# Optimization experiments

Hardware: AMD Instinct MI355X
Metric: run time of the kernel (lower is better)

The kernel has to match this reference:

```python
import jax, jax.numpy as jnp
import numpy as np

B, S, H = 2, 1024, 2048
NH, NKV, D = 16, 4, 128
E, K, F = 16, 2, 1408          # routed experts, top_k, moe_intermediate
FS = 1408                      # shared-expert intermediate (n_shared_experts=1)
EPS = 1e-5
RSF = 1.0                      # routed_scaling_factor


def rmsnorm(x, w):
    v = jnp.mean(jnp.square(x.astype(jnp.float32)), axis=-1, keepdims=True)
    return (x * jax.lax.rsqrt(v + EPS)).astype(x.dtype) * w


def rotate_half(x):
    x1, x2 = jnp.split(x, 2, axis=-1)
    return jnp.concatenate([-x2, x1], axis=-1)


def apply_rope(x, cos, sin):
    # x: [B,S,h,D]; cos/sin: [S,D]
    c = cos[None, :, None, :]
    s = sin[None, :, None, :]
    return x * c + rotate_half(x) * s


def setup_inputs() -> dict:
    key = jax.random.key(0)
    ks = jax.random.split(key, 16)
    sc = 0.02
    hidden_states = jax.random.normal(ks[0], (B, S, H), dtype=jnp.float32)
    # rotary embedding tables
    inv_freq = 1.0 / (10000.0 ** (np.arange(0, D, 2, dtype=np.float32) / D))
    ang = np.arange(S, dtype=np.float32)[:, None] * inv_freq[None, :]
    emb = np.concatenate([ang, ang], axis=-1)
    cos = jnp.asarray(np.cos(emb), dtype=jnp.float32)
    sin = jnp.asarray(np.sin(emb), dtype=jnp.float32)
    return {
        'hidden_states': hidden_states,
        'cos': cos,
        'sin': sin,
        'ln1_w': jnp.ones((H,), jnp.float32),
        'ln2_w': jnp.ones((H,), jnp.float32),
        'q_norm_w': jnp.ones((D,), jnp.float32),
        'k_norm_w': jnp.ones((D,), jnp.float32),
        'wq': jax.random.normal(ks[1], (H, NH * D), jnp.float32) * sc,
        'wk': jax.random.normal(ks[2], (H, NKV * D), jnp.float32) * sc,
        'wv': jax.random.normal(ks[3], (H, NKV * D), jnp.float32) * sc,
        'wo': jax.random.normal(ks[4], (NH * D, H), jnp.float32) * sc,
        'gate_w': jax.random.normal(ks[5], (E, H), jnp.float32) * sc,
        'expert_gate_up': jax.random.normal(ks[6], (E, H, 2 * F), jnp.float32) * sc,
        'expert_down': jax.random.normal(ks[7], (E, F, H), jnp.float32) * sc,
        'shared_gate_up': jax.random.normal(ks[8], (H, 2 * FS), jnp.float32) * sc,
        'shared_down': jax.random.normal(ks[9], (FS, H), jnp.float32) * sc,
    }


def silu_and_mul(gu):
    g, u = jnp.split(gu, 2, axis=-1)
    return jax.nn.silu(g) * u


def moe_block(tokens, gate_w, expert_gate_up, expert_down, shared_gate_up, shared_down):
    # tokens: [T,H]
    T = tokens.shape[0]
    router_logits = tokens.astype(jnp.float32) @ gate_w.T          # [T,E]
    probs = jax.nn.softmax(router_logits, axis=-1)
    topk_w, topk_ids = jax.lax.top_k(probs, K)                     # [T,K]
    topk_w = topk_w / jnp.sum(topk_w, axis=-1, keepdims=True)      # renormalize
    # dense combine-weight matrix [T,E] (top_k sparse routing)
    cw = jnp.zeros((T, E), jnp.float32).at[jnp.arange(T)[:, None], topk_ids].add(topk_w)
    # scan over experts: each expert is a full SwiGLU MLP on all tokens, masked by cw
    def body(acc, we):
        gw, dw, cwe = we                                            # [H,2F],[F,H],[T]
        y = silu_and_mul(tokens @ gw) @ dw                          # [T,H]
        return acc + cwe[:, None].astype(y.dtype) * y, None
    out, _ = jax.lax.scan(body, jnp.zeros_like(tokens), (expert_gate_up, expert_down, cw.T))
    out = out * RSF
    shared = silu_and_mul(tokens @ shared_gate_up) @ shared_down
    return out + shared


def reference(hidden_states, cos, sin, ln1_w, ln2_w, q_norm_w, k_norm_w,
              wq, wk, wv, wo, gate_w, expert_gate_up, expert_down,
              shared_gate_up, shared_down):
    # input layernorm (residual=None branch)
    residual = hidden_states
    x = rmsnorm(hidden_states, ln1_w)
    # attention
    q = (x @ wq).reshape(B, S, NH, D)
    k = (x @ wk).reshape(B, S, NKV, D)
    v = (x @ wv).reshape(B, S, NKV, D)
    q = rmsnorm(q, q_norm_w)
    k = rmsnorm(k, k_norm_w)
    q = apply_rope(q, cos, sin)
    k = apply_rope(k, cos, sin)
    rep = NH // NKV
    k = jnp.repeat(k, rep, axis=2)
    v = jnp.repeat(v, rep, axis=2)
    scores = jnp.einsum('bihd,bjhd->bhij', q, k) / jnp.sqrt(jnp.float32(D))
    causal = jnp.tril(jnp.ones((S, S), bool))
    scores = jnp.where(causal[None, None], scores, -jnp.inf)
    attn = jax.nn.softmax(scores, axis=-1)
    o = jnp.einsum('bhij,bjhd->bihd', attn, v).reshape(B, S, NH * D)
    attn_out = o @ wo
    # post-attention layernorm with fused residual add
    residual = residual + attn_out
    x = rmsnorm(residual, ln2_w)
    # MoE + shared expert
    tokens = x.reshape(-1, H)
    out = moe_block(tokens, gate_w, expert_gate_up, expert_down, shared_gate_up, shared_down)
    hidden = out.reshape(B, S, H)
    return hidden, residual
```

## Files before the change

kernel.cpp:

```cpp
#include <hip/hip_runtime.h>
#include <stdint.h>

typedef unsigned short u16;
typedef unsigned int   u32;
typedef __attribute__((ext_vector_type(4))) float     f32x4;
typedef __attribute__((ext_vector_type(8))) _Float16  f16x8;

#define S_LEN 1024
#define NB    2
#define H_DIM 2048
#define T_TOK 2048
#define NHEAD 16
#define NKVH  4
#define DHEAD 128
#define NEXP  16
#define FFE   1408
#define FF2   2816
#define EPSF  1e-5f
#define RSF_C 1.0f

__device__ __forceinline__ u16 f2h(float f){
  _Float16 h = (_Float16)f;
  return __builtin_bit_cast(unsigned short, h);
}
__device__ __forceinline__ void split2(float f, u16& hi, u16& lo){
  _Float16 h = (_Float16)f;
  hi = __builtin_bit_cast(unsigned short, h);
  _Float16 l = (_Float16)((f - (float)h) * 2048.0f);
  lo = __builtin_bit_cast(unsigned short, l);
}
__device__ __forceinline__ void gload_lds16(const void* g, void* l){
  __builtin_amdgcn_global_load_lds((const __attribute__((address_space(1))) void*)g,
                                   (__attribute__((address_space(3))) void*)l, 16, 0, 0);
}
__device__ __forceinline__ uint4 pack8(const u16* p){
  return make_uint4((u32)p[0] | ((u32)p[1]<<16), (u32)p[2] | ((u32)p[3]<<16),
                    (u32)p[4] | ((u32)p[5]<<16), (u32)p[6] | ((u32)p[7]<<16));
}

template<bool DUAL>
__global__ __launch_bounds__(256) void tsplit_kernel(
    const float* __restrict__ in, int ldn,
    u16* __restrict__ outh, u16* __restrict__ outl, int ldk)
{
  __shared__ float tile[64][65];
  const int n0 = blockIdx.x * 64, k0 = blockIdx.y * 64;
  const int tid = threadIdx.x;
  const int tr = tid >> 4, tc = (tid & 15) * 4;
  #pragma unroll
  for (int i = 0; i < 4; i++) {
    float4 v = *(const float4*)&in[(size_t)(k0 + tr + i*16) * ldn + (n0 + tc)];
    tile[tr + i*16][tc+0] = v.x; tile[tr + i*16][tc+1] = v.y;
    tile[tr + i*16][tc+2] = v.z; tile[tr + i*16][tc+3] = v.w;
  }
  __syncthreads();
  const int n = tid >> 2, kg = (tid & 3) * 16;
  u16 hb[16], lb[16];
  #pragma unroll
  for (int j = 0; j < 16; j++) {
    float f = tile[kg + j][n];
    if (DUAL) split2(f, hb[j], lb[j]); else hb[j] = f2h(f);
  }
  u16* dh = &outh[(size_t)(n0 + n) * ldk + k0 + kg];
  *(uint4*)dh       = pack8(hb);
  *(uint4*)(dh + 8) = pack8(hb + 8);
  if (DUAL) {
    u16* dl = &outl[(size_t)(n0 + n) * ldk + k0 + kg];
    *(uint4*)dl       = pack8(lb);
    *(uint4*)(dl + 8) = pack8(lb + 8);
  }
}

__global__ __launch_bounds__(256) void rmsnorm_kernel(
    const float* __restrict__ in, const float* __restrict__ w,
    u16* __restrict__ outh, u16* __restrict__ outl)
{
  __shared__ float red[4];
  const int t = blockIdx.x, tid = threadIdx.x;
  const int lane = tid & 63, wave = tid >> 6;
  const float* x = in + (size_t)t * H_DIM;
  const int c = tid * 8;
  float4 v0 = *(const float4*)&x[c];
  float4 v1 = *(const float4*)&x[c + 4];
  float ss = v0.x*v0.x + v0.y*v0.y + v0.z*v0.z + v0.w*v0.w
           + v1.x*v1.x + v1.y*v1.y + v1.z*v1.z + v1.w*v1.w;
  #pragma unroll
  for (int d = 1; d < 64; d <<= 1) ss += __shfl_xor(ss, d, 64);
  if (lane == 0) red[wave] = ss;
  __syncthreads();
  float rinv = rsqrtf((red[0]+red[1]+red[2]+red[3]) * (1.0f/H_DIM) + EPSF);
  float4 w0 = *(const float4*)&w[c];
  float4 w1 = *(const float4*)&w[c + 4];
  float vals[8] = { v0.x*rinv*w0.x, v0.y*rinv*w0.y, v0.z*rinv*w0.z, v0.w*rinv*w0.w,
                    v1.x*rinv*w1.x, v1.y*rinv*w1.y, v1.z*rinv*w1.z, v1.w*rinv*w1.w };
  u16 hb[8], lb[8];
  #pragma unroll
  for (int j = 0; j < 8; j++) split2(vals[j], hb[j], lb[j]);
  *(uint4*)&outh[(size_t)t * H_DIM + c] = pack8(hb);
  if (outl) *(uint4*)&outl[(size_t)t * H_DIM + c] = pack8(lb);
}

__global__ __launch_bounds__(256) void gemm3b_kernel(
    const u16* __restrict__ Ah, const u16* __restrict__ Al, int lda,
    const u16* __restrict__ Bh, const u16* __restrict__ Bl, int ldb,
    float* __restrict__ C, int ldc,
    const float* __restrict__ addsrc, int K)
{
  __shared__ u16 Ash[128*64], Asl[128*64];
  __shared__ u16 Bsh[128*64], Bsl[128*64];
  const int tid = threadIdx.x, lane = tid & 63, wave = tid >> 6;
  const int m0 = blockIdx.y * 128, n0 = blockIdx.x * 128;
  const int wm = (wave >> 1) * 64, wn = (wave & 1) * 64;
  const int arow = lane >> 3;
  const int acol = ((lane & 7) ^ arow) * 8;
  f32x4 acc0[4][4] = {}, acc1[4][4] = {};
  for (int k0 = 0; k0 < K; k0 += 64) {
    #pragma unroll
    for (int g = 0; g < 4; g++) {
      const int rb = wave*32 + g*8;
      gload_lds16(Ah + (size_t)(m0 + rb + arow)*lda + k0 + acol, &Ash[rb*64]);
      gload_lds16(Al + (size_t)(m0 + rb + arow)*lda + k0 + acol, &Asl[rb*64]);
      gload_lds16(Bh + (size_t)(n0 + rb + arow)*ldb + k0 + acol, &Bsh[rb*64]);
      gload_lds16(Bl + (size_t)(n0 + rb + arow)*ldb + k0 + acol, &Bsl[rb*64]);
    }
    asm volatile("s_waitcnt vmcnt(0) lgkmcnt(0)" ::: "memory");
    __syncthreads();
    const int fr = lane & 15, fg = lane >> 4;
    #pragma unroll
    for (int kk = 0; kk < 2; kk++) {
      const int cb = fg + kk*4;
      f16x8 ah[4], al[4];
      #pragma unroll
      for (int m = 0; m < 4; m++) {
        const int r = wm + m*16 + fr;
        const int s = (cb ^ (r & 7)) * 8;
        ah[m] = *(const f16x8*)&Ash[r*64 + s];
        al[m] = *(const f16x8*)&Asl[r*64 + s];
      }
      #pragma unroll
      for (int n = 0; n < 4; n++) {
        const int r = wn + n*16 + fr;
        const int s = (cb ^ (r & 7)) * 8;
        f16x8 bh_ = *(const f16x8*)&Bsh[r*64 + s];
        f16x8 bl_ = *(const f16x8*)&Bsl[r*64 + s];
        #pragma unroll
        for (int m = 0; m < 4; m++) {
          acc0[m][n] = __builtin_amdgcn_mfma_f32_16x16x32_f16(ah[m], bh_, acc0[m][n], 0,0,0);
          acc1[m][n] = __builtin_amdgcn_mfma_f32_16x16x32_f16(ah[m], bl_, acc1[m][n], 0,0,0);
          acc1[m][n] = __builtin_amdgcn_mfma_f32_16x16x32_f16(al[m], bh_, acc1[m][n], 0,0,0);
        }
      }
    }
    __syncthreads();
  }
  const int cr = (lane >> 4) * 4, cc = lane & 15;
  #pragma unroll
  for (int m = 0; m < 4; m++)
    #pragma unroll
    for (int n = 0; n < 4; n++)
      #pragma unroll
      for (int j = 0; j < 4; j++) {
        int r = m0 + wm + m*16 + cr + j;
        size_t idx = (size_t)r * ldc + (n0 + wn + n*16 + cc);
        float v = acc0[m][n][j] + acc1[m][n][j] * (1.0f/2048.0f);
        if (addsrc) v += addsrc[idx];
        C[idx] = v;
      }
}

template<int KCH>
__global__ __launch_bounds__(256) void gemm_s_kernel(
    const u16* __restrict__ A, int lda,
    const u16* __restrict__ B, int ldb,
    float* __restrict__ C, int ldc, int Ktot)
{
  __shared__ u16 As[128*64], Bs[128*64];
  const int tid = threadIdx.x, lane = tid & 63, wave = tid >> 6;
  const int m0 = blockIdx.y * 128, n0 = blockIdx.x * 128;
  const int klen = Ktot / KCH;
  const int kbeg = blockIdx.z * klen, kend = kbeg + klen;
  const int wm = (wave >> 1) * 64, wn = (wave & 1) * 64;
  const int arow = lane >> 3;
  const int acol = ((lane & 7) ^ arow) * 8;
  f32x4 acc[4][4] = {};
  for (int k0 = kbeg; k0 < kend; k0 += 64) {
    #pragma unroll
    for (int g = 0; g < 4; g++) {
      const int rb = wave*32 + g*8;
      gload_lds16(A + (size_t)(m0 + rb + arow)*lda + k0 + acol, &As[rb*64]);
      gload_lds16(B + (size_t)(n0 + rb + arow)*ldb + k0 + acol, &Bs[rb*64]);
    }
    asm volatile("s_waitcnt vmcnt(0) lgkmcnt(0)" ::: "memory");
    __syncthreads();
    const int fr = lane & 15, fg = lane >> 4;
    #pragma unroll
    for (int kk = 0; kk < 2; kk++) {
      const int cb = fg + kk*4;
      f16x8 a[4];
      #pragma unroll
      for (int m = 0; m < 4; m++) {
        const int r = wm + m*16 + fr;
        a[m] = *(const f16x8*)&As[r*64 + ((cb ^ (r & 7)) * 8)];
      }
      #pragma unroll
      for (int n = 0; n < 4; n++) {
        const int r = wn + n*16 + fr;
        f16x8 b_ = *(const f16x8*)&Bs[r*64 + ((cb ^ (r & 7)) * 8)];
        #pragma unroll
        for (int m = 0; m < 4; m++)
          acc[m][n] = __builtin_amdgcn_mfma_f32_16x16x32_f16(a[m], b_, acc[m][n], 0,0,0);
      }
    }
    __syncthreads();
  }
  const int cr = (lane >> 4) * 4, cc = lane & 15;
  #pragma unroll
  for (int m = 0; m < 4; m++)
    #pragma unroll
    for (int n = 0; n < 4; n++)
      #pragma unroll
      for (int j = 0; j < 4; j++) {
        size_t idx = (size_t)(m0 + wm + m*16 + cr + j) * ldc + (n0 + wn + n*16 + cc);
        if (KCH == 1) C[idx] = acc[m][n][j];
        else          atomicAdd(&C[idx], acc[m][n][j]);
      }
}

__global__ __launch_bounds__(256) void gemm_s64_kernel(
    const u16* __restrict__ A, int lda,
    const u16* __restrict__ B, int ldb,
    float* __restrict__ C, int ldc, int Ktot)
{
  __shared__ u16 As[256*64];
  __shared__ u16 Bs[64*64];
  const int tid = threadIdx.x, lane = tid & 63, wave = tid >> 6;
  const int m0 = blockIdx.y * 256, n0 = blockIdx.x * 64;
  const int wm = wave * 64;
  const int arow = lane >> 3;
  const int acol = ((lane & 7) ^ arow) * 8;
  f32x4 acc[4][4] = {};
  for (int k0 = 0; k0 < Ktot; k0 += 64) {
    #pragma unroll
    for (int g = 0; g < 8; g++)
      gload_lds16(A + (size_t)(m0 + wm + g*8 + arow)*lda + k0 + acol,
                  &As[(wm + g*8)*64]);
    #pragma unroll
    for (int g = 0; g < 2; g++)
      gload_lds16(B + (size_t)(n0 + wave*16 + g*8 + arow)*ldb + k0 + acol,
                  &Bs[(wave*16 + g*8)*64]);
    asm volatile("s_waitcnt vmcnt(0) lgkmcnt(0)" ::: "memory");
    __syncthreads();
    const int fr = lane & 15, fg = lane >> 4;
    #pragma unroll
    for (int kk = 0; kk < 2; kk++) {
      const int cb = fg + kk*4;
      f16x8 a[4], b[4];
      #pragma unroll
      for (int m = 0; m < 4; m++) {
        const int r = wm + m*16 + fr;
        a[m] = *(const f16x8*)&As[r*64 + ((cb ^ (r & 7)) * 8)];
      }
      #pragma unroll
      for (int n = 0; n < 4; n++) {
        const int r = n*16 + fr;
        b[n] = *(const f16x8*)&Bs[r*64 + ((cb ^ (r & 7)) * 8)];
      }
      #pragma unroll
      for (int n = 0; n < 4; n++)
        #pragma unroll
        for (int m = 0; m < 4; m++)
          acc[m][n] = __builtin_amdgcn_mfma_f32_16x16x32_f16(a[m], b[n], acc[m][n], 0,0,0);
    }
    __syncthreads();
  }
  const int cr = (lane >> 4) * 4, cc = lane & 15;
  #pragma unroll
  for (int m = 0; m < 4; m++)
    #pragma unroll
    for (int n = 0; n < 4; n++)
      #pragma unroll
      for (int j = 0; j < 4; j++) {
        size_t idx = (size_t)(m0 + wm + m*16 + cr + j) * ldc + (n0 + n*16 + cc);
        C[idx] = acc[m][n][j];
      }
}

template<int KCH>
__global__ __launch_bounds__(256) void gemm_e_kernel(
    const u16* __restrict__ Abase, int lda,
    const float* __restrict__ Bbase, int ldb, size_t bstride,
    float* __restrict__ Cbase, int ldc,
    const int* __restrict__ counts, const int* __restrict__ offs,
    const int* __restrict__ tile_e, const int* __restrict__ tile_m0, int Ktot)
{
  __shared__ u16 As[256*64];
  __shared__ u16 Bs[64*64];
  const int tile = blockIdx.z / KCH, kc = blockIdx.z % KCH;
  const int e = tile_e[tile];
  if (e < 0) return;
  const int m0 = tile_m0[tile];
  const int cnt = counts[e];
  const int off = offs[e];
  const u16* A = Abase + (size_t)off * lda;
  const float* B = Bbase + bstride * (size_t)e;
  float* C = Cbase + (size_t)off * ldc;
  const int tid = threadIdx.x, lane = tid & 63, wave = tid >> 6;
  const int n0 = blockIdx.x * 64;
  const int wm = wave * 64;
  const int arow = lane >> 3;
  const int acol = ((lane & 7) ^ arow) * 8;
  const int bn  = tid & 63;
  const int bkb = tid >> 6;
  const int bs0 = bn*64 + (((bkb*2)     ^ (bn & 7)) * 8);
  const int bs1 = bn*64 + (((bkb*2 + 1) ^ (bn & 7)) * 8);
  const int klen = Ktot / KCH;
  const int kbeg = kc * klen, kend = kbeg + klen;
  f32x4 acc[4][4] = {};
  for (int k0 = kbeg; k0 < kend; k0 += 64) {
    #pragma unroll
    for (int g = 0; g < 8; g++)
      gload_lds16(A + (size_t)(m0 + wm + g*8 + arow)*lda + k0 + acol,
                  &As[(wm + g*8)*64]);
    {
      const float* gb = B + (size_t)(k0 + bkb*16) * ldb + (n0 + bn);
      float f[16];
      #pragma unroll
      for (int j = 0; j < 16; j++) f[j] = gb[(size_t)j * ldb];
      u32 pk[8];
      #pragma unroll
      for (int j = 0; j < 8; j++)
        pk[j] = __builtin_bit_cast(u32, __builtin_amdgcn_cvt_pkrtz(f[2*j], f[2*j+1]));
      *(uint4*)&Bs[bs0] = make_uint4(pk[0], pk[1], pk[2], pk[3]);
      *(uint4*)&Bs[bs1] = make_uint4(pk[4], pk[5], pk[6], pk[7]);
    }
    asm volatile("s_waitcnt vmcnt(0) lgkmcnt(0)" ::: "memory");
    __syncthreads();
    const int fr = lane & 15, fg = lane >> 4;
    #pragma unroll
    for (int kk = 0; kk < 2; kk++) {
      const int cb = fg + kk*4;
      f16x8 a[4], b[4];
      #pragma unroll
      for (int m = 0; m < 4; m++) {
        const int r = wm + m*16 + fr;
        a[m] = *(const f16x8*)&As[r*64 + ((cb ^ (r & 7)) * 8)];
      }
      #pragma unroll
      for (int n = 0; n < 4; n++) {
        const int r = n*16 + fr;
        b[n] = *(const f16x8*)&Bs[r*64 + ((cb ^ (r & 7)) * 8)];
      }
      #pragma unroll
      for (int n = 0; n < 4; n++)
        #pragma unroll
        for (int m = 0; m < 4; m++)
          acc[m][n] = __builtin_amdgcn_mfma_f32_16x16x32_f16(a[m], b[n], acc[m][n], 0,0,0);
    }
    __syncthreads();
  }
  const int cr = (lane >> 4) * 4, cc = lane & 15;
  #pragma unroll
  for (int m = 0; m < 4; m++)
    #pragma unroll
    for (int n = 0; n < 4; n++)
      #pragma unroll
      for (int j = 0; j < 4; j++) {
        int r = m0 + wm + m*16 + cr + j;
        if (r < cnt) {
          size_t idx = (size_t)r * ldc + (n0 + n*16 + cc);
          if (KCH == 1) C[idx] = acc[m][n][j];
          else          atomicAdd(&C[idx], acc[m][n][j]);
        }
      }
}

__global__ __launch_bounds__(256) void rope_kernel(
    const float* __restrict__ qkv,
    const float* __restrict__ cosb, const float* __restrict__ sinb,
    const float* __restrict__ qnw, const float* __restrict__ knw,
    u16* __restrict__ qrh, u16* __restrict__ qrl,
    u16* __restrict__ krh, u16* __restrict__ krl,
    u16* __restrict__ vth, u16* __restrict__ vtl)
{
  const int jid = blockIdx.x * 4 + (threadIdx.x >> 6);
  const int lane = threadIdx.x & 63;
  const int t = jid / 24, r = jid - t*24;
  const int b = t >> 10, s = t & (S_LEN - 1);
  const float* row = qkv + (size_t)t * 3072;
  if (r < NHEAD + NKVH) {
    const bool isq = (r < NHEAD);
    const int h = isq ? r : (r - NHEAD);
    const float* x = row + (isq ? h*DHEAD : (2048 + h*DHEAD));
    const float* nw = isq ? qnw : knw;
    float x0 = x[lane], x1 = x[lane + 64];
    float ss = x0*x0 + x1*x1;
    #pragma unroll
    for (int d = 1; d < 64; d <<= 1) ss += __shfl_xor(ss, d, 64);
    float rinv = rsqrtf(ss * (1.0f/DHEAD) + EPSF);
    float n0 = x0*rinv*nw[lane], n1 = x1*rinv*nw[lane + 64];
    float o0 = n0*cosb[s*DHEAD + lane]      - n1*sinb[s*DHEAD + lane];
    float o1 = n1*cosb[s*DHEAD + lane + 64] + n0*sinb[s*DHEAD + lane + 64];
    size_t base = isq ? ((size_t)(b*NHEAD + h)*S_LEN + s)*DHEAD
                      : ((size_t)(b*NKVH + h)*S_LEN + s)*DHEAD;
    u16* dh = isq ? qrh : krh;
    u16* dl = isq ? qrl : krl;
    u16 hh, ll;
    split2(o0, hh, ll); dh[base + lane]      = hh; dl[base + lane]      = ll;
    split2(o1, hh, ll); dh[base + lane + 64] = hh; dl[base + lane + 64] = ll;
  } else {
    const int h = r - NHEAD - NKVH;
    const float* x = row + 2560 + h*DHEAD;
    size_t base = (size_t)(b*NKVH + h)*DHEAD*S_LEN + s;
    u16 hh, ll;
    split2(x[lane], hh, ll);
    vth[base + (size_t)lane*S_LEN] = hh; vtl[base + (size_t)lane*S_LEN] = ll;
    split2(x[lane + 64], hh, ll);
    vth[base + (size_t)(lane + 64)*S_LEN] = hh; vtl[base + (size_t)(lane + 64)*S_LEN] = ll;
  }
}

__global__ __launch_bounds__(256) void attn_kernel(
    const u16* __restrict__ qrh, const u16* __restrict__ qrl,
    const u16* __restrict__ krh, const u16* __restrict__ krl,
    const u16* __restrict__ vth, const u16* __restrict__ vtl,
    u16* __restrict__ oh, u16* __restrict__ ol)
{
  __shared__ u16 Kh[64*128], Kl[64*128];
  __shared__ u16 Vh[128*64], Vl[128*64];
  __shared__ u16 Ph[4*16*64], Pl[4*16*64];
  const int bx = blockIdx.x, h = blockIdx.y, b = blockIdx.z;
  const int hkv = h >> 2;
  const int lane = threadIdx.x & 63, wave = threadIdx.x >> 6;
  const int fr = lane & 15, fg = lane >> 4;
  const u16* qbh = qrh + ((size_t)(b*NHEAD + h)*S_LEN)*DHEAD;
  const u16* qbl = qrl + ((size_t)(b*NHEAD + h)*S_LEN)*DHEAD;
  const u16* kbh = krh + ((size_t)(b*NKVH + hkv)*S_LEN)*DHEAD;
  const u16* kbl = krl + ((size_t)(b*NKVH + hkv)*S_LEN)*DHEAD;
  const u16* vbh = vth + ((size_t)(b*NKVH + hkv)*DHEAD)*S_LEN;
  const u16* vbl = vtl + ((size_t)(b*NKVH + hkv)*DHEAD)*S_LEN;
  const float scl = 0.08838834764831845f;

  for (int it = 0; it < 2; it++) {
    const int qt = it ? (15 - bx) : bx;
    const int q0 = qt * 64;
    f16x8 aqh[4], aql[4];
    {
      const size_t qrow = (size_t)(q0 + wave*16 + fr)*DHEAD;
      #pragma unroll
      for (int kk = 0; kk < 4; kk++) {
        aqh[kk] = *(const f16x8*)&qbh[qrow + kk*32 + fg*8];
        aql[kk] = *(const f16x8*)&qbl[qrow + kk*32 + fg*8];
      }
    }
    f32x4 o0[8] = {}, o1[8] = {};
    float mrow[4] = {-1e30f,-1e30f,-1e30f,-1e30f};
    float lrow[4] = {0.f,0.f,0.f,0.f};
// ... 111 lines not shown
  float xv[32];
  float ss = 0.f;
  #pragma unroll
  for (int p = 0; p < 8; p++) {
    float4 v  = *(const float4*)&x[p*256 + lane*4];
    float4 lw = *(const float4*)&ln2w[p*256 + lane*4];
    ss += v.x*v.x + v.y*v.y + v.z*v.z + v.w*v.w;
    xv[p*4+0] = v.x*lw.x; xv[p*4+1] = v.y*lw.y; xv[p*4+2] = v.z*lw.z; xv[p*4+3] = v.w*lw.w;
  }
  #pragma unroll
  for (int d = 1; d < 64; d <<= 1) ss += __shfl_xor(ss, d, 64);
  const float rinv = rsqrtf(ss * (1.0f/H_DIM) + EPSF);
  float lg[NEXP];
  #pragma unroll
  for (int e = 0; e < NEXP; e++) {
    const float* g = gw + (size_t)e * H_DIM;
    float dacc = 0.f;
    #pragma unroll
    for (int p = 0; p < 8; p++) {
      float4 gv = *(const float4*)&g[p*256 + lane*4];
      dacc += xv[p*4+0]*gv.x + xv[p*4+1]*gv.y + xv[p*4+2]*gv.z + xv[p*4+3]*gv.w;
    }
    #pragma unroll
    for (int d = 1; d < 64; d <<= 1) dacc += __shfl_xor(dacc, d, 64);
    lg[e] = dacc * rinv;
  }
  if (lane == 0) {
    int i0 = 0; float b0 = lg[0];
    #pragma unroll
    for (int e = 1; e < NEXP; e++) if (lg[e] > b0) { b0 = lg[e]; i0 = e; }
    int i1 = -1; float b1 = -3e38f;
    #pragma unroll
    for (int e = 0; e < NEXP; e++) if (e != i0 && lg[e] > b1) { b1 = lg[e]; i1 = e; }
    float rr = __expf(b1 - b0);
    float w0 = 1.0f / (1.0f + rr);
    ids[t*2] = i0; ids[t*2+1] = i1;
    wts[t*2] = w0; wts[t*2+1] = rr * w0;
    atomicAdd(&counts[i0], 1);
    atomicAdd(&counts[i1], 1);
  }
}

__global__ void scan_kernel(const int* __restrict__ counts, int* __restrict__ offs,
                            int* __restrict__ cursor,
                            int* __restrict__ tile_e, int* __restrict__ tile_m0)
{
  if (threadIdx.x == 0) {
    int s = 0, nt = 0;
    for (int e = 0; e < NEXP; e++) {
      offs[e] = s; cursor[e] = 0;
      int c = counts[e];
      for (int m0 = 0; m0 < c; m0 += 256) { tile_e[nt] = e; tile_m0[nt] = m0; nt++; }
      s += c;
    }
    for (; nt < 32; nt++) { tile_e[nt] = -1; tile_m0[nt] = 0; }
  }
}

__global__ __launch_bounds__(256) void scatter_kernel(
    const int* __restrict__ ids, const int* __restrict__ offs,
    int* __restrict__ cursor, int* __restrict__ list, int* __restrict__ pos)
{
  int t = blockIdx.x * 256 + threadIdx.x;
  if (t < T_TOK) {
    for (int kk = 0; kk < 2; kk++) {
      int e = ids[t*2 + kk];
      int p = atomicAdd(&cursor[e], 1);
      int i = offs[e] + p;
      list[i] = t;
      pos[t*2 + kk] = i;
    }
  }
}

__global__ __launch_bounds__(256) void gather_kernel(
    const u16* __restrict__ tok, const int* __restrict__ list, u16* __restrict__ aexp)
{
  const int i = blockIdx.x;
  const int t = list[i];
  const int c = threadIdx.x * 8;
  *(uint4*)&aexp[(size_t)i*H_DIM + c] = *(const uint4*)&tok[(size_t)t*H_DIM + c];
}

__global__ __launch_bounds__(256) void silu_kernel(
    const float* __restrict__ gu, u16* __restrict__ act)
{
  const int rr = blockIdx.x;
  const float* g = gu + (size_t)rr * FF2;
  u16* o = act + (size_t)rr * FFE;
  for (int c = threadIdx.x*4; c < FFE; c += 1024) {
    float4 gv = *(const float4*)&g[c];
    float4 uv = *(const float4*)&g[c + FFE];
    float s0 = gv.x / (1.0f + __expf(-gv.x)) * uv.x;
    float s1 = gv.y / (1.0f + __expf(-gv.y)) * uv.y;
    float s2 = gv.z / (1.0f + __expf(-gv.z)) * uv.z;
    float s3 = gv.w / (1.0f + __expf(-gv.w)) * uv.w;
    u32 lo = (u32)f2h(s0) | ((u32)f2h(s1) << 16);
    u32 hi = (u32)f2h(s2) | ((u32)f2h(s3) << 16);
    *(uint2*)&o[c] = make_uint2(lo, hi);
  }
}

__global__ __launch_bounds__(256) void combine_kernel(
    const float* __restrict__ y,
    const int* __restrict__ pos, const float* __restrict__ wts,
    float* __restrict__ out)
{
  const int t = blockIdx.x;
  const int p0 = pos[t*2], p1 = pos[t*2+1];
  const float w0 = wts[t*2] * RSF_C, w1 = wts[t*2+1] * RSF_C;
  const int c = threadIdx.x * 8;
  #pragma unroll
  for (int q = 0; q < 2; q++) {
    const int cc = c + q*4;
    float4 s  = *(const float4*)&out[(size_t)t*H_DIM + cc];
    float4 a  = *(const float4*)&y[(size_t)p0*H_DIM + cc];
    float4 bb = *(const float4*)&y[(size_t)p1*H_DIM + cc];
    float4 r;
    r.x = s.x + w0*a.x + w1*bb.x;
    r.y = s.y + w0*a.y + w1*bb.y;
    r.z = s.z + w0*a.z + w1*bb.z;
    r.w = s.w + w0*a.w + w1*bb.w;
    *(float4*)&out[(size_t)t*H_DIM + cc] = r;
  }
}

extern "C" void kernel_launch(void* const* d_in, const int* in_sizes, int n_in,
                              void* d_out, int out_size, void* d_ws, size_t ws_size,
                              hipStream_t stream)
{
  (void)in_sizes; (void)n_in; (void)out_size;
  const float* hidden = (const float*)d_in[0];
  const float* cosb   = (const float*)d_in[1];
  const float* sinb   = (const float*)d_in[2];
  const float* ln1w   = (const float*)d_in[3];
  const float* ln2w   = (const float*)d_in[4];
  const float* qnw    = (const float*)d_in[5];
  const float* knw    = (const float*)d_in[6];
  const float* wq     = (const float*)d_in[7];
  const float* wk     = (const float*)d_in[8];
  const float* wv     = (const float*)d_in[9];
  const float* wo     = (const float*)d_in[10];
  const float* gw     = (const float*)d_in[11];
  const float* egu    = (const float*)d_in[12];
  const float* edn    = (const float*)d_in[13];
  const float* sgu    = (const float*)d_in[14];
  const float* sdn    = (const float*)d_in[15];
  float* out_hidden = (float*)d_out;
  float* resid = (float*)d_out + (size_t)T_TOK * H_DIM;

  char* ws = (char*)d_ws;
  constexpr size_t OFF_XH    = 0;
  constexpr size_t OFF_XL    = 8388608;
  constexpr size_t OFF_WQKVH = 16777216;
  constexpr size_t OFF_WQKVL = 29360128;
  constexpr size_t OFF_WOH   = 41943040;
  constexpr size_t OFF_WOL   = 50331648;
  constexpr size_t OFF_QKV   = 58720256;
  constexpr size_t OFF_QRH = 16777216, OFF_QRL = 25165824;
  constexpr size_t OFF_KRH = 33554432, OFF_KRL = 35651584;
  constexpr size_t OFF_VTH = 37748736, OFF_VTL = 39845888;
  constexpr size_t OFF_OH = 58720256, OFF_OL = 67108864;
  constexpr size_t OFF_GUE = 0;
  constexpr size_t OFF_AEX = 46137344;
  constexpr size_t OFF_TOK = 63963136;
  constexpr size_t OFF_ACE = 72351744;
  constexpr size_t OFF_GUS = 84606976;
  constexpr size_t OFF_ACS = 107675648;
  constexpr size_t OFF_SGUT= 113442816;
  constexpr size_t OFF_SDNT= 124977152;
  constexpr size_t OFF_IDS = 130744320;
  constexpr size_t OFF_WTS = OFF_IDS + 16384;
  constexpr size_t OFF_POS = OFF_WTS + 16384;
  constexpr size_t OFF_LST = OFF_POS + 16384;
  constexpr size_t OFF_CNT = OFF_LST + 16384;
  constexpr size_t OFF_OFS = OFF_CNT + 64;
  constexpr size_t OFF_CUR = OFF_OFS + 64;
  constexpr size_t OFF_TE  = OFF_CUR + 64;
  constexpr size_t OFF_TM  = OFF_TE + 128;
  constexpr size_t WS_NEED = OFF_TM + 128;
  if (ws_size < WS_NEED) return;

  u16* xh     = (u16*)(ws + OFF_XH);
  u16* xl     = (u16*)(ws + OFF_XL);
  u16* wqkvh  = (u16*)(ws + OFF_WQKVH);
  u16* wqkvl  = (u16*)(ws + OFF_WQKVL);
  u16* woh    = (u16*)(ws + OFF_WOH);
  u16* wol    = (u16*)(ws + OFF_WOL);
  float* qkv  = (float*)(ws + OFF_QKV);
  u16* q_rh = (u16*)(ws + OFF_QRH);
  u16* q_rl = (u16*)(ws + OFF_QRL);
  u16* k_rh = (u16*)(ws + OFF_KRH);
  u16* k_rl = (u16*)(ws + OFF_KRL);
  u16* v_th = (u16*)(ws + OFF_VTH);
  u16* v_tl = (u16*)(ws + OFF_VTL);
  u16* o_h  = (u16*)(ws + OFF_OH);
  u16* o_l  = (u16*)(ws + OFF_OL);
  float* gu_exp = (float*)(ws + OFF_GUE);
  float* y_exp  = (float*)(ws + OFF_GUE);
  u16* a_exp    = (u16*)(ws + OFF_AEX);
  u16* tok      = (u16*)(ws + OFF_TOK);
  u16* act_ex   = (u16*)(ws + OFF_ACE);
  float* gu_sh  = (float*)(ws + OFF_GUS);
  u16* act_sh   = (u16*)(ws + OFF_ACS);
  u16* sgut     = (u16*)(ws + OFF_SGUT);
  u16* sdnt     = (u16*)(ws + OFF_SDNT);
  int* ids    = (int*)(ws + OFF_IDS);
  float* wts  = (float*)(ws + OFF_WTS);
  int* pos    = (int*)(ws + OFF_POS);
  int* list   = (int*)(ws + OFF_LST);
  int* counts = (int*)(ws + OFF_CNT);
  int* offs   = (int*)(ws + OFF_OFS);
  int* cursor = (int*)(ws + OFF_CUR);
  int* tile_e = (int*)(ws + OFF_TE);
  int* tile_m0= (int*)(ws + OFF_TM);

  hipMemsetAsync(counts, 0, 64, stream);

  tsplit_kernel<true><<<dim3(32,32), 256, 0, stream>>>(wq, 2048, wqkvh,              wqkvl,              2048);
  tsplit_kernel<true><<<dim3(8,32),  256, 0, stream>>>(wk, 512,  wqkvh + 2048*2048,  wqkvl + 2048*2048,  2048);
  tsplit_kernel<true><<<dim3(8,32),  256, 0, stream>>>(wv, 512,  wqkvh + 2560*2048,  wqkvl + 2560*2048,  2048);
  tsplit_kernel<true><<<dim3(32,32), 256, 0, stream>>>(wo, 2048, woh, wol, 2048);
  tsplit_kernel<false><<<dim3(44,32),256, 0, stream>>>(sgu, 2816, sgut, nullptr, 2048);
  tsplit_kernel<false><<<dim3(32,22),256, 0, stream>>>(sdn, 2048, sdnt, nullptr, 1408);

  rmsnorm_kernel<<<T_TOK, 256, 0, stream>>>(hidden, ln1w, xh, xl);
  gemm3b_kernel<<<dim3(24,16), 256, 0, stream>>>(xh, xl, H_DIM, wqkvh, wqkvl, 2048, qkv, 3072, nullptr, H_DIM);
  rope_kernel<<<(T_TOK*24)/4, 256, 0, stream>>>(qkv, cosb, sinb, qnw, knw,
                                                q_rh, q_rl, k_rh, k_rl, v_th, v_tl);
  attn_kernel<<<dim3(8, NHEAD, NB), 256, 0, stream>>>(q_rh, q_rl, k_rh, k_rl, v_th, v_tl, o_h, o_l);
  gemm3b_kernel<<<dim3(16,16), 256, 0, stream>>>(o_h, o_l, H_DIM, woh, wol, 2048, resid, H_DIM, hidden, H_DIM);

  rmsnorm_kernel<<<T_TOK, 256, 0, stream>>>(resid, ln2w, tok, nullptr);
  router_kernel<<<T_TOK, 64, 0, stream>>>(resid, ln2w, gw, ids, wts, counts);
  scan_kernel<<<1, 64, 0, stream>>>(counts, offs, cursor, tile_e, tile_m0);
  scatter_kernel<<<8, 256, 0, stream>>>(ids, offs, cursor, list, pos);
  gather_kernel<<<2*T_TOK, 256, 0, stream>>>(tok, list, a_exp);

  gemm_s64_kernel<<<dim3(44,8,1), 256, 0, stream>>>(tok, H_DIM, sgut, 2048, gu_sh, FF2, H_DIM);
  silu_kernel<<<T_TOK, 256, 0, stream>>>(gu_sh, act_sh);
  gemm_s_kernel<1><<<dim3(16,16,1), 256, 0, stream>>>(act_sh, FFE, sdnt, FFE, out_hidden, H_DIM, FFE);

  gemm_e_kernel<1><<<dim3(44,1,32), 256, 0, stream>>>(a_exp, H_DIM, egu, FF2, (size_t)H_DIM*FF2,
                                                      gu_exp, FF2, counts, offs, tile_e, tile_m0, H_DIM);
  silu_kernel<<<2*T_TOK, 256, 0, stream>>>(gu_exp, act_ex);
  gemm_e_kernel<1><<<dim3(32,1,32), 256, 0, stream>>>(act_ex, FFE, edn, H_DIM, (size_t)FFE*H_DIM,
                                                      y_exp, H_DIM, counts, offs, tile_e, tile_m0, FFE);
  combine_kernel<<<T_TOK, 256, 0, stream>>>(y_exp, pos, wts, out_hidden);
}
```

Baseline: 803.7 us.

## Merge expert and shared-expert GEMMs, SiLU, and weight transposes into single launches

Six weight-transpose launches become one grid that uses blockIdx.z to pick the matrix. The shared-expert and routed-expert up and down GEMMs are combined into single launches, with z<32 handling expert tiles and z>=32 handling shared tiles. SiLU for both paths runs in one kernel. This cuts launch count and lets the shared and routed GEMMs share the GPU instead of running back to back; the shared down GEMM now uses the 256x64 tile shape instead of 128x128. The runtime dual flag and the many idle blocks in the padded transpose grid add a little overhead.

Result: faster. 746.8 us (-7.1%).

```diff
diff --git a/kernel.cpp b/kernel.cpp
--- a/kernel.cpp
+++ b/kernel.cpp
@@ -38,11 +38,25 @@
                     (u32)p[4] | ((u32)p[5]<<16), (u32)p[6] | ((u32)p[7]<<16));
 }
 
-template<bool DUAL>
-__global__ __launch_bounds__(256) void tsplit_kernel(
-    const float* __restrict__ in, int ldn,
-    u16* __restrict__ outh, u16* __restrict__ outl, int ldk)
-{
+__global__ __launch_bounds__(256) void tsplit_all_kernel(
+    const float* __restrict__ wq, const float* __restrict__ wk,
+    const float* __restrict__ wv, const float* __restrict__ wo,
+    const float* __restrict__ sgu, const float* __restrict__ sdn,
+    u16* __restrict__ wqkvh, u16* __restrict__ wqkvl,
+    u16* __restrict__ woh,  u16* __restrict__ wol,
+    u16* __restrict__ sgut, u16* __restrict__ sdnt)
+{
+  const int z = blockIdx.z;
+  const float* in; int ldn; u16* outh; u16* outl; int ldk, nx, ny; bool dual;
+  switch (z) {
+    case 0:  in=wq;  ldn=2048; outh=wqkvh;              outl=wqkvl;              ldk=2048; nx=32; ny=32; dual=true;  break;
+    case 1:  in=wk;  ldn=512;  outh=wqkvh+2048*2048;    outl=wqkvl+2048*2048;    ldk=2048; nx=8;  ny=32; dual=true;  break;
+    case 2:  in=wv;  ldn=512;  outh=wqkvh+2560*2048;    outl=wqkvl+2560*2048;    ldk=2048; nx=8;  ny=32; dual=true;  break;
+    case 3:  in=wo;  ldn=2048; outh=woh;                outl=wol;                ldk=2048; nx=32; ny=32; dual=true;  break;
+    case 4:  in=sgu; ldn=2816; outh=sgut;               outl=nullptr;            ldk=2048; nx=44; ny=32; dual=false; break;
+    default: in=sdn; ldn=2048; outh=sdnt;               outl=nullptr;            ldk=1408; nx=32; ny=22; dual=false; break;
+  }
+  if ((int)blockIdx.x >= nx || (int)blockIdx.y >= ny) return;
   __shared__ float tile[64][65];
   const int n0 = blockIdx.x * 64, k0 = blockIdx.y * 64;
   const int tid = threadIdx.x;
@@ -59,12 +73,12 @@
   #pragma unroll
   for (int j = 0; j < 16; j++) {
     float f = tile[kg + j][n];
-    if (DUAL) split2(f, hb[j], lb[j]); else hb[j] = f2h(f);
+    if (dual) split2(f, hb[j], lb[j]); else hb[j] = f2h(f);
   }
   u16* dh = &outh[(size_t)(n0 + n) * ldk + k0 + kg];
   *(uint4*)dh       = pack8(hb);
   *(uint4*)(dh + 8) = pack8(hb + 8);
-  if (DUAL) {
+  if (dual) {
     u16* dl = &outl[(size_t)(n0 + n) * ldk + k0 + kg];
     *(uint4*)dl       = pack8(lb);
     *(uint4*)(dl + 8) = pack8(lb + 8);
@@ -168,210 +182,258 @@
       }
 }
 
-template<int KCH>
-__global__ __launch_bounds__(256) void gemm_s_kernel(
-    const u16* __restrict__ A, int lda,
-    const u16* __restrict__ B, int ldb,
-    float* __restrict__ C, int ldc, int Ktot)
-{
-  __shared__ u16 As[128*64], Bs[128*64];
-  const int tid = threadIdx.x, lane = tid & 63, wave = tid >> 6;
-  const int m0 = blockIdx.y * 128, n0 = blockIdx.x * 128;
-  const int klen = Ktot / KCH;
-  const int kbeg = blockIdx.z * klen, kend = kbeg + klen;
-  const int wm = (wave >> 1) * 64, wn = (wave & 1) * 64;
-  const int arow = lane >> 3;
-  const int acol = ((lane & 7) ^ arow) * 8;
-  f32x4 acc[4][4] = {};
-  for (int k0 = kbeg; k0 < kend; k0 += 64) {
-    #pragma unroll
-    for (int g = 0; g < 4; g++) {
-      const int rb = wave*32 + g*8;
-      gload_lds16(A + (size_t)(m0 + rb + arow)*lda + k0 + acol, &As[rb*64]);
-      gload_lds16(B + (size_t)(n0 + rb + arow)*ldb + k0 + acol, &Bs[rb*64]);
-    }
-    asm volatile("s_waitcnt vmcnt(0) lgkmcnt(0)" ::: "memory");
-    __syncthreads();
-    const int fr = lane & 15, fg = lane >> 4;
-    #pragma unroll
-    for (int kk = 0; kk < 2; kk++) {
-      const int cb = fg + kk*4;
-      f16x8 a[4];
-      #pragma unroll
-      for (int m = 0; m < 4; m++) {
-        const int r = wm + m*16 + fr;
-        a[m] = *(const f16x8*)&As[r*64 + ((cb ^ (r & 7)) * 8)];
-      }
-      #pragma unroll
-      for (int n = 0; n < 4; n++) {
-        const int r = wn + n*16 + fr;
-        f16x8 b_ = *(const f16x8*)&Bs[r*64 + ((cb ^ (r & 7)) * 8)];
-        #pragma unroll
-        for (int m = 0; m < 4; m++)
-          acc[m][n] = __builtin_amdgcn_mfma_f32_16x16x32_f16(a[m], b_, acc[m][n], 0,0,0);
-      }
-    }
-    __syncthreads();
-  }
-  const int cr = (lane >> 4) * 4, cc = lane & 15;
-  #pragma unroll
-  for (int m = 0; m < 4; m++)
-    #pragma unroll
-    for (int n = 0; n < 4; n++)
-      #pragma unroll
-      for (int j = 0; j < 4; j++) {
-        size_t idx = (size_t)(m0 + wm + m*16 + cr + j) * ldc + (n0 + wn + n*16 + cc);
-        if (KCH == 1) C[idx] = acc[m][n][j];
-        else          atomicAdd(&C[idx], acc[m][n][j]);
-      }
-}
-
-__global__ __launch_bounds__(256) void gemm_s64_kernel(
-    const u16* __restrict__ A, int lda,
-    const u16* __restrict__ B, int ldb,
-    float* __restrict__ C, int ldc, int Ktot)
+__global__ __launch_bounds__(256) void gemm_up_all_kernel(
+    const u16* __restrict__ Aexp, const float* __restrict__ egu, float* __restrict__ gu_exp,
+    const int* __restrict__ counts, const int* __restrict__ offs,
+    const int* __restrict__ tile_e, const int* __restrict__ tile_m0,
+    const u16* __restrict__ tok, const u16* __restrict__ sgut, float* __restrict__ gu_sh)
 {
   __shared__ u16 As[256*64];
   __shared__ u16 Bs[64*64];
-  const int tid = threadIdx.x, lane = tid & 63, wave = tid >> 6;
-  const int m0 = blockIdx.y * 256, n0 = blockIdx.x * 64;
-  const int wm = wave * 64;
-  const int arow = lane >> 3;
-  const int acol = ((lane & 7) ^ arow) * 8;
-  f32x4 acc[4][4] = {};
-  for (int k0 = 0; k0 < Ktot; k0 += 64) {
-    #pragma unroll
-    for (int g = 0; g < 8; g++)
-      gload_lds16(A + (size_t)(m0 + wm + g*8 + arow)*lda + k0 + acol,
-                  &As[(wm + g*8)*64]);
-    #pragma unroll
-    for (int g = 0; g < 2; g++)
-      gload_lds16(B + (size_t)(n0 + wave*16 + g*8 + arow)*ldb + k0 + acol,
-                  &Bs[(wave*16 + g*8)*64]);
-    asm volatile("s_waitcnt vmcnt(0) lgkmcnt(0)" ::: "memory");
-    __syncthreads();
-    const int fr = lane & 15, fg = lane >> 4;
-    #pragma unroll
-    for (int kk = 0; kk < 2; kk++) {
-      const int cb = fg + kk*4;
-      f16x8 a[4], b[4];
-      #pragma unroll
-      for (int m = 0; m < 4; m++) {
-        const int r = wm + m*16 + fr;
-        a[m] = *(const f16x8*)&As[r*64 + ((cb ^ (r & 7)) * 8)];
-      }
-      #pragma unroll
-      for (int n = 0; n < 4; n++) {
-        const int r = n*16 + fr;
-        b[n] = *(const f16x8*)&Bs[r*64 + ((cb ^ (r & 7)) * 8)];
-      }
-      #pragma unroll
-      for (int n = 0; n < 4; n++)
-        #pragma unroll
-        for (int m = 0; m < 4; m++)
-          acc[m][n] = __builtin_amdgcn_mfma_f32_16x16x32_f16(a[m], b[n], acc[m][n], 0,0,0);
-    }
-    __syncthreads();
-  }
-  const int cr = (lane >> 4) * 4, cc = lane & 15;
-  #pragma unroll
-  for (int m = 0; m < 4; m++)
-    #pragma unroll
-    for (int n = 0; n < 4; n++)
-      #pragma unroll
-      for (int j = 0; j < 4; j++) {
-        size_t idx = (size_t)(m0 + wm + m*16 + cr + j) * ldc + (n0 + n*16 + cc);
-        C[idx] = acc[m][n][j];
-      }
-}
-
-template<int KCH>
-__global__ __launch_bounds__(256) void gemm_e_kernel(
-    const u16* __restrict__ Abase, int lda,
-    const float* __restrict__ Bbase, int ldb, size_t bstride,
-    float* __restrict__ Cbase, int ldc,
-    const int* __restrict__ counts, const int* __restrict__ offs,
-    const int* __restrict__ tile_e, const int* __restrict__ tile_m0, int Ktot)
-{
-  __shared__ u16 As[256*64];
-  __shared__ u16 Bs[64*64];
-  const int tile = blockIdx.z / KCH, kc = blockIdx.z % KCH;
-  const int e = tile_e[tile];
-  if (e < 0) return;
-  const int m0 = tile_m0[tile];
-  const int cnt = counts[e];
-  const int off = offs[e];
-  const u16* A = Abase + (size_t)off * lda;
-  const float* B = Bbase + bstride * (size_t)e;
-  float* C = Cbase + (size_t)off * ldc;
+  const int z = blockIdx.z;
   const int tid = threadIdx.x, lane = tid & 63, wave = tid >> 6;
   const int n0 = blockIdx.x * 64;
   const int wm = wave * 64;
   const int arow = lane >> 3;
   const int acol = ((lane & 7) ^ arow) * 8;
-  const int bn  = tid & 63;
-  const int bkb = tid >> 6;
-  const int bs0 = bn*64 + (((bkb*2)     ^ (bn & 7)) * 8);
-  const int bs1 = bn*64 + (((bkb*2 + 1) ^ (bn & 7)) * 8);
-  const int klen = Ktot / KCH;
-  const int kbeg = kc * klen, kend = kbeg + klen;
-  f32x4 acc[4][4] = {};
-  for (int k0 = kbeg; k0 < kend; k0 += 64) {
-    #pragma unroll
-    for (int g = 0; g < 8; g++)
-      gload_lds16(A + (size_t)(m0 + wm + g*8 + arow)*lda + k0 + acol,
-                  &As[(wm + g*8)*64]);
-    {
-      const float* gb = B + (size_t)(k0 + bkb*16) * ldb + (n0 + bn);
-      float f[16];
-      #pragma unroll
-      for (int j = 0; j < 16; j++) f[j] = gb[(size_t)j * ldb];
-      u32 pk[8];
-      #pragma unroll
-      for (int j = 0; j < 8; j++)
-        pk[j] = __builtin_bit_cast(u32, __builtin_amdgcn_cvt_pkrtz(f[2*j], f[2*j+1]));
-      *(uint4*)&Bs[bs0] = make_uint4(pk[0], pk[1], pk[2], pk[3]);
-      *(uint4*)&Bs[bs1] = make_uint4(pk[4], pk[5], pk[6], pk[7]);
-    }
-    asm volatile("s_waitcnt vmcnt(0) lgkmcnt(0)" ::: "memory");
-    __syncthreads();
-    const int fr = lane & 15, fg = lane >> 4;
-    #pragma unroll
-    for (int kk = 0; kk < 2; kk++) {
-      const int cb = fg + kk*4;
-      f16x8 a[4], b[4];
-      #pragma unroll
-      for (int m = 0; m < 4; m++) {
-        const int r = wm + m*16 + fr;
-        a[m] = *(const f16x8*)&As[r*64 + ((cb ^ (r & 7)) * 8)];
-      }
-      #pragma unroll
-      for (int n = 0; n < 4; n++) {
-        const int r = n*16 + fr;
-        b[n] = *(const f16x8*)&Bs[r*64 + ((cb ^ (r & 7)) * 8)];
-      }
+  const int fr = lane & 15, fg = lane >> 4;
+  const int cr = (lane >> 4) * 4, cc = lane & 15;
+
+  if (z < 32) {
+    const int e = tile_e[z];
+    if (e < 0) return;
+    const int m0 = tile_m0[z];
+    const int cnt = counts[e];
+    const int off = offs[e];
+    const u16* A = Aexp + (size_t)off * H_DIM;
+    const float* B = egu + (size_t)e * H_DIM * FF2;
+    float* C = gu_exp + (size_t)off * FF2;
+    const int bn  = tid & 63;
+    const int bkb = tid >> 6;
+    const int bs0 = bn*64 + (((bkb*2)     ^ (bn & 7)) * 8);
+    const int bs1 = bn*64 + (((bkb*2 + 1) ^ (bn & 7)) * 8);
+    f32x4 acc[4][4] = {};
+    for (int k0 = 0; k0 < H_DIM; k0 += 64) {
+      #pragma unroll
+      for (int g = 0; g < 8; g++)
+        gload_lds16(A + (size_t)(m0 + wm + g*8 + arow)*H_DIM + k0 + acol,
+                    &As[(wm + g*8)*64]);
+      {
+        const float* gb = B + (size_t)(k0 + bkb*16) * FF2 + (n0 + bn);
+        float f[16];
+        #pragma unroll
+        for (int j = 0; j < 16; j++) f[j] = gb[(size_t)j * FF2];
+        u32 pk[8];
+        #pragma unroll
+        for (int j = 0; j < 8; j++)
+          pk[j] = __builtin_bit_cast(u32, __builtin_amdgcn_cvt_pkrtz(f[2*j], f[2*j+1]));
+        *(uint4*)&Bs[bs0] = make_uint4(pk[0], pk[1], pk[2], pk[3]);
+        *(uint4*)&Bs[bs1] = make_uint4(pk[4], pk[5], pk[6], pk[7]);
+      }
+      asm volatile("s_waitcnt vmcnt(0) lgkmcnt(0)" ::: "memory");
+      __syncthreads();
+      #pragma unroll
+      for (int kk = 0; kk < 2; kk++) {
+        const int cb = fg + kk*4;
+        f16x8 a[4], b[4];
+        #pragma unroll
+        for (int m = 0; m < 4; m++) {
+          const int r = wm + m*16 + fr;
+          a[m] = *(const f16x8*)&As[r*64 + ((cb ^ (r & 7)) * 8)];
+        }
+        #pragma unroll
+        for (int n = 0; n < 4; n++) {
+          const int r = n*16 + fr;
+          b[n] = *(const f16x8*)&Bs[r*64 + ((cb ^ (r & 7)) * 8)];
+        }
+        #pragma unroll
+        for (int n = 0; n < 4; n++)
+          #pragma unroll
+          for (int m = 0; m < 4; m++)
+            acc[m][n] = __builtin_amdgcn_mfma_f32_16x16x32_f16(a[m], b[n], acc[m][n], 0,0,0);
+      }
+      __syncthreads();
+    }
+    #pragma unroll
+    for (int m = 0; m < 4; m++)
       #pragma unroll
       for (int n = 0; n < 4; n++)
         #pragma unroll
-        for (int m = 0; m < 4; m++)
-          acc[m][n] = __builtin_amdgcn_mfma_f32_16x16x32_f16(a[m], b[n], acc[m][n], 0,0,0);
-    }
-    __syncthreads();
-  }
+        for (int j = 0; j < 4; j++) {
+          int r = m0 + wm + m*16 + cr + j;
+          if (r < cnt) C[(size_t)r * FF2 + (n0 + n*16 + cc)] = acc[m][n][j];
+        }
+  } else {
+    const int m0 = (z - 32) * 256;
+    f32x4 acc[4][4] = {};
+    for (int k0 = 0; k0 < H_DIM; k0 += 64) {
+      #pragma unroll
+      for (int g = 0; g < 8; g++)
+        gload_lds16(tok + (size_t)(m0 + wm + g*8 + arow)*H_DIM + k0 + acol,
+                    &As[(wm + g*8)*64]);
+      #pragma unroll
+      for (int g = 0; g < 2; g++)
+        gload_lds16(sgut + (size_t)(n0 + wave*16 + g*8 + arow)*H_DIM + k0 + acol,
+                    &Bs[(wave*16 + g*8)*64]);
+      asm volatile("s_waitcnt vmcnt(0) lgkmcnt(0)" ::: "memory");
+      __syncthreads();
+      #pragma unroll
+      for (int kk = 0; kk < 2; kk++) {
+        const int cb = fg + kk*4;
+        f16x8 a[4], b[4];
+        #pragma unroll
+        for (int m = 0; m < 4; m++) {
+          const int r = wm + m*16 + fr;
+          a[m] = *(const f16x8*)&As[r*64 + ((cb ^ (r & 7)) * 8)];
+        }
+        #pragma unroll
+        for (int n = 0; n < 4; n++) {
+          const int r = n*16 + fr;
+          b[n] = *(const f16x8*)&Bs[r*64 + ((cb ^ (r & 7)) * 8)];
+        }
+        #pragma unroll
+        for (int n = 0; n < 4; n++)
+          #pragma unroll
+          for (int m = 0; m < 4; m++)
+            acc[m][n] = __builtin_amdgcn_mfma_f32_16x16x32_f16(a[m], b[n], acc[m][n], 0,0,0);
+      }
+      __syncthreads();
+    }
+    #pragma unroll
+    for (int m = 0; m < 4; m++)
+      #pragma unroll
+      for (int n = 0; n < 4; n++)
+        #pragma unroll
+        for (int j = 0; j < 4; j++)
+          gu_sh[(size_t)(m0 + wm + m*16 + cr + j) * FF2 + (n0 + n*16 + cc)] = acc[m][n][j];
+  }
+}
+
+__global__ __launch_bounds__(256) void gemm_dn_all_kernel(
+    const u16* __restrict__ Aexp, const float* __restrict__ edn, float* __restrict__ y_exp,
+    const int* __restrict__ counts, const int* __restrict__ offs,
+    const int* __restrict__ tile_e, const int* __restrict__ tile_m0,
+    const u16* __restrict__ act_sh, const u16* __restrict__ sdnt, float* __restrict__ out_sh)
+{
+  __shared__ u16 As[256*64];
+  __shared__ u16 Bs[64*64];
+  const int z = blockIdx.z;
+  const int tid = threadIdx.x, lane = tid & 63, wave = tid >> 6;
+  const int n0 = blockIdx.x * 64;
+  const int wm = wave * 64;
+  const int arow = lane >> 3;
+  const int acol = ((lane & 7) ^ arow) * 8;
+  const int fr = lane & 15, fg = lane >> 4;
   const int cr = (lane >> 4) * 4, cc = lane & 15;
-  #pragma unroll
-  for (int m = 0; m < 4; m++)
-    #pragma unroll
-    for (int n = 0; n < 4; n++)
-      #pragma unroll
-      for (int j = 0; j < 4; j++) {
-        int r = m0 + wm + m*16 + cr + j;
-        if (r < cnt) {
-          size_t idx = (size_t)r * ldc + (n0 + n*16 + cc);
-          if (KCH == 1) C[idx] = acc[m][n][j];
-          else          atomicAdd(&C[idx], acc[m][n][j]);
-        }
-      }
+
+  if (z < 32) {
+    const int e = tile_e[z];
+    if (e < 0) return;
+    const int m0 = tile_m0[z];
+    const int cnt = counts[e];
+    const int off = offs[e];
+    const u16* A = Aexp + (size_t)off * FFE;
+    const float* B = edn + (size_t)e * FFE * H_DIM;
+    float* C = y_exp + (size_t)off * H_DIM;
+    const int bn  = tid & 63;
+    const int bkb = tid >> 6;
+    const int bs0 = bn*64 + (((bkb*2)     ^ (bn & 7)) * 8);
+    const int bs1 = bn*64 + (((bkb*2 + 1) ^ (bn & 7)) * 8);
+    f32x4 acc[4][4] = {};
+    for (int k0 = 0; k0 < FFE; k0 += 64) {
+      #pragma unroll
+      for (int g = 0; g < 8; g++)
+        gload_lds16(A + (size_t)(m0 + wm + g*8 + arow)*FFE + k0 + acol,
+                    &As[(wm + g*8)*64]);
+      {
+        const float* gb = B + (size_t)(k0 + bkb*16) * H_DIM + (n0 + bn);
+        float f[16];
+        #pragma unroll
+        for (int j = 0; j < 16; j++) f[j] = gb[(size_t)j * H_DIM];
+        u32 pk[8];
+        #pragma unroll
+        for (int j = 0; j < 8; j++)
+          pk[j] = __builtin_bit_cast(u32, __builtin_amdgcn_cvt_pkrtz(f[2*j], f[2*j+1]));
+        *(uint4*)&Bs[bs0] = make_uint4(pk[0], pk[1], pk[2], pk[3]);
+        *(uint4*)&Bs[bs1] = make_uint4(pk[4], pk[5], pk[6], pk[7]);
+      }
+      asm volatile("s_waitcnt vmcnt(0) lgkmcnt(0)" ::: "memory");
+      __syncthreads();
+      #pragma unroll
+      for (int kk = 0; kk < 2; kk++) {
+        const int cb = fg + kk*4;
+        f16x8 a[4], b[4];
+        #pragma unroll
+        for (int m = 0; m < 4; m++) {
+          const int r = wm + m*16 + fr;
+          a[m] = *(const f16x8*)&As[r*64 + ((cb ^ (r & 7)) * 8)];
+        }
+        #pragma unroll
+        for (int n = 0; n < 4; n++) {
+          const int r = n*16 + fr;
+          b[n] = *(const f16x8*)&Bs[r*64 + ((cb ^ (r & 7)) * 8)];
+        }
+        #pragma unroll
+        for (int n = 0; n < 4; n++)
+          #pragma unroll
+          for (int m = 0; m < 4; m++)
+            acc[m][n] = __builtin_amdgcn_mfma_f32_16x16x32_f16(a[m], b[n], acc[m][n], 0,0,0);
+      }
+      __syncthreads();
+    }
+    #pragma unroll
+    for (int m = 0; m < 4; m++)
+      #pragma unroll
+      for (int n = 0; n < 4; n++)
+        #pragma unroll
+        for (int j = 0; j < 4; j++) {
+          int r = m0 + wm + m*16 + cr + j;
+          if (r < cnt) C[(size_t)r * H_DIM + (n0 + n*16 + cc)] = acc[m][n][j];
+        }
+  } else {
+    const int m0 = (z - 32) * 256;
+    f32x4 acc[4][4] = {};
+    for (int k0 = 0; k0 < FFE; k0 += 64) {
+      #pragma unroll
+      for (int g = 0; g < 8; g++)
+        gload_lds16(act_sh + (size_t)(m0 + wm + g*8 + arow)*FFE + k0 + acol,
+                    &As[(wm + g*8)*64]);
+      #pragma unroll
+      for (int g = 0; g < 2; g++)
+        gload_lds16(sdnt + (size_t)(n0 + wave*16 + g*8 + arow)*FFE + k0 + acol,
+                    &Bs[(wave*16 + g*8)*64]);
+      asm volatile("s_waitcnt vmcnt(0) lgkmcnt(0)" ::: "memory");
+      __syncthreads();
+      #pragma unroll
+      for (int kk = 0; kk < 2; kk++) {
+        const int cb = fg + kk*4;
+        f16x8 a[4], b[4];
+        #pragma unroll
+        for (int m = 0; m < 4; m++) {
+          const int r = wm + m*16 + fr;
+          a[m] = *(const f16x8*)&As[r*64 + ((cb ^ (r & 7)) * 8)];
+        }
+        #pragma unroll
+        for (int n = 0; n < 4; n++) {
+          const int r = n*16 + fr;
+          b[n] = *(const f16x8*)&Bs[r*64 + ((cb ^ (r & 7)) * 8)];
+        }
+        #pragma unroll
+        for (int n = 0; n < 4; n++)
+          #pragma unroll
+          for (int m = 0; m < 4; m++)
+            acc[m][n] = __builtin_amdgcn_mfma_f32_16x16x32_f16(a[m], b[n], acc[m][n], 0,0,0);
+      }
+      __syncthreads();
+    }
+    #pragma unroll
+    for (int m = 0; m < 4; m++)
+      #pragma unroll
+      for (int n = 0; n < 4; n++)
+        #pragma unroll
+        for (int j = 0; j < 4; j++)
+          out_sh[(size_t)(m0 + wm + m*16 + cr + j) * H_DIM + (n0 + n*16 + cc)] = acc[m][n][j];
+  }
 }
 
 __global__ __launch_bounds__(256) void rope_kernel(
@@ -649,12 +711,15 @@
   *(uint4*)&aexp[(size_t)i*H_DIM + c] = *(const uint4*)&tok[(size_t)t*H_DIM + c];
 }
 
-__global__ __launch_bounds__(256) void silu_kernel(
-    const float* __restrict__ gu, u16* __restrict__ act)
+__global__ __launch_bounds__(256) void silu_all_kernel(
+    const float* __restrict__ gu_exp, u16* __restrict__ act_ex,
+    const float* __restrict__ gu_sh,  u16* __restrict__ act_sh)
 {
   const int rr = blockIdx.x;
-  const float* g = gu + (size_t)rr * FF2;
-  u16* o = act + (size_t)rr * FFE;
+  const float* g;
+  u16* o;
+  if (rr < 2*T_TOK) { g = gu_exp + (size_t)rr * FF2;          o = act_ex + (size_t)rr * FFE; }
+  else              { g = gu_sh  + (size_t)(rr - 2*T_TOK) * FF2; o = act_sh + (size_t)(rr - 2*T_TOK) * FFE; }
   for (int c = threadIdx.x*4; c < FFE; c += 1024) {
     float4 gv = *(const float4*)&g[c];
     float4 uv = *(const float4*)&g[c + FFE];
@@ -784,12 +849,8 @@
 
   hipMemsetAsync(counts, 0, 64, stream);
 
-  tsplit_kernel<true><<<dim3(32,32), 256, 0, stream>>>(wq, 2048, wqkvh,              wqkvl,              2048);
-  tsplit_kernel<true><<<dim3(8,32),  256, 0, stream>>>(wk, 512,  wqkvh + 2048*2048,  wqkvl + 2048*2048,  2048);
-  tsplit_kernel<true><<<dim3(8,32),  256, 0, stream>>>(wv, 512,  wqkvh + 2560*2048,  wqkvl + 2560*2048,  2048);
-  tsplit_kernel<true><<<dim3(32,32), 256, 0, stream>>>(wo, 2048, woh, wol, 2048);
-  tsplit_kernel<false><<<dim3(44,32),256, 0, stream>>>(sgu, 2816, sgut, nullptr, 2048);
-  tsplit_kernel<false><<<dim3(32,22),256, 0, stream>>>(sdn, 2048, sdnt, nullptr, 1408);
+  tsplit_all_kernel<<<dim3(44,32,6), 256, 0, stream>>>(wq, wk, wv, wo, sgu, sdn,
+                                                       wqkvh, wqkvl, woh, wol, sgut, sdnt);
 
   rmsnorm_kernel<<<T_TOK, 256, 0, stream>>>(hidden, ln1w, xh, xl);
   gemm3b_kernel<<<dim3(24,16), 256, 0, stream>>>(xh, xl, H_DIM, wqkvh, wqkvl, 2048, qkv, 3072, nullptr, H_DIM);
@@ -804,14 +865,12 @@
   scatter_kernel<<<8, 256, 0, stream>>>(ids, offs, cursor, list, pos);
   gather_kernel<<<2*T_TOK, 256, 0, stream>>>(tok, list, a_exp);
 
-  gemm_s64_kernel<<<dim3(44,8,1), 256, 0, stream>>>(tok, H_DIM, sgut, 2048, gu_sh, FF2, H_DIM);
-  silu_kernel<<<T_TOK, 256, 0, stream>>>(gu_sh, act_sh);
-  gemm_s_kernel<1><<<dim3(16,16,1), 256, 0, stream>>>(act_sh, FFE, sdnt, FFE, out_hidden, H_DIM, FFE);
-
-  gemm_e_kernel<1><<<dim3(44,1,32), 256, 0, stream>>>(a_exp, H_DIM, egu, FF2, (size_t)H_DIM*FF2,
-                                                      gu_exp, FF2, counts, offs, tile_e, tile_m0, H_DIM);
-  silu_kernel<<<2*T_TOK, 256, 0, stream>>>(gu_exp, act_ex);
-  gemm_e_kernel<1><<<dim3(32,1,32), 256, 0, stream>>>(act_ex, FFE, edn, H_DIM, (size_t)FFE*H_DIM,
-                                                      y_exp, H_DIM, counts, offs, tile_e, tile_m0, FFE);
+  gemm_up_all_kernel<<<dim3(44,1,40), 256, 0, stream>>>(a_exp, egu, gu_exp,
+                                                        counts, offs, tile_e, tile_m0,
+                                                        tok, sgut, gu_sh);
+  silu_all_kernel<<<3*T_TOK, 256, 0, stream>>>(gu_exp, act_ex, gu_sh, act_sh);
+  gemm_dn_all_kernel<<<dim3(32,1,40), 256, 0, stream>>>(act_ex, edn, y_exp,
+                                                        counts, offs, tile_e, tile_m0,
+                                                        act_sh, sdnt, out_hidden);
   combine_kernel<<<T_TOK, 256, 0, stream>>>(y_exp, pos, wts, out_hidden);
 }
```
